# Optimization experiments

Hardware: AMD Instinct MI355X
Metric: run time of the kernel (lower is better)

The kernel has to match this reference:

```python
import jax, jax.numpy as jnp
import numpy as np

D_IN, D_HID = 64, 128

def _ff(x, w1, b1, w2, b2):
    # FeedForward: Linear -> ReLU -> Linear
    return jax.nn.relu(x @ w1 + b1) @ w2 + b2

def setup_inputs() -> dict:
    key = jax.random.key(0)
    ks = jax.random.split(key, 10)
    N, m = 8, 2048
    def lin(k, fan_in, fan_out):
        bound = 1.0 / np.sqrt(fan_in)
        return jax.random.uniform(k, (fan_in, fan_out), jnp.float32, -bound, bound)
    return {
        "x": jax.random.normal(ks[0], (N, m, D_IN), jnp.float32),
        "edge": jax.random.uniform(ks[1], (N, m, m), jnp.float32),
        # f: dim_in -> dim_hid//2 -> dim_hid
        "f_w1": lin(ks[2], D_IN, D_HID // 2),
        "f_b1": jnp.zeros((D_HID // 2,), jnp.float32),
        "f_w2": lin(ks[3], D_HID // 2, D_HID),
        "f_b2": jnp.zeros((D_HID,), jnp.float32),
        # g: 2*dim_in -> dim_hid -> dim_hid
        "g_w1": lin(ks[4], 2 * D_IN, D_HID),
        "g_b1": jnp.zeros((D_HID,), jnp.float32),
        "g_w2": lin(ks[5], D_HID, D_HID),
        "g_b2": jnp.zeros((D_HID,), jnp.float32),
    }

def reference(x, edge, f_w1, f_b1, f_w2, f_b2, g_w1, g_b1, g_w2, g_b2):
    # self dynamics: f(x) -> [N, m, D_HID]
    self_dyn = _ff(x, f_w1, f_b1, f_w2, f_b2)
    # Original builds interaction[n,i,j] = cat(x[n,i], x[n,i]) (receiver is
    # transposed twice), so g is constant along j. Compute g once per sender node.
    gx = _ff(jnp.concatenate([x, x], axis=-1), g_w1, g_b1, g_w2, g_b2)  # [N, m, H]
    # interaction.sum over sender dim i with edge weights: out[n,j] = sum_i edge[n,i,j]*gx[n,i]
    inter = jnp.einsum('nij,nih->njh', edge, gx)
    return self_dyn + inter
```

## Files before the change

kernel.cpp:

```cpp
#include <hip/hip_runtime.h>


typedef __attribute__((ext_vector_type(8))) short bf16x8;
typedef __attribute__((ext_vector_type(4))) unsigned short u16x4;
typedef __attribute__((ext_vector_type(4))) float f32x4;

static __device__ __forceinline__ unsigned short f2bf(float f) {
  union { float f; unsigned int i; } c; c.f = f;
  return (unsigned short)((c.i + 0x7fffu + ((c.i >> 16) & 1u)) >> 16);
}

__global__ __launch_bounds__(256) void k_gx(
    const float* __restrict__ x,
    const float* __restrict__ gw1,
    const float* __restrict__ gb1,
    const float* __restrict__ gw2,
    const float* __restrict__ gb2,
    unsigned short* __restrict__ gxT)
{
  __shared__ short xs[64 * 64];
  __shared__ short w1T[128 * 64];
  __shared__ short w2T[128 * 128];
  __shared__ short h2s[64 * 128];

  const int t = threadIdx.x;
  const int R0 = blockIdx.x * 64;

  for (int idx = t; idx < 64 * 128; idx += 256) {
    int k = idx >> 7, n = idx & 127;
    float v = gw1[idx] + gw1[64 * 128 + idx];
    w1T[(n << 6) + (((k >> 3) ^ (n & 7)) << 3) + (k & 7)] = (short)f2bf(v);
  }
  for (int idx = t; idx < 128 * 128; idx += 256) {
    int k = idx >> 7, n = idx & 127;
    w2T[(n << 7) + (((k >> 3) ^ (n & 7)) << 3) + (k & 7)] = (short)f2bf(gw2[idx]);
  }
  for (int s = t; s < 64 * 16; s += 256) {
    int row = s >> 4, c4 = s & 15;
    f32x4 v = *(const f32x4*)(x + (size_t)(R0 + row) * 64 + c4 * 4);
    u16x4 pk;
#pragma unroll
    for (int r = 0; r < 4; ++r) pk[r] = f2bf(v[r]);
    *(u16x4*)(xs + (row << 6) + (((c4 >> 1) ^ (row & 7)) << 3) + ((c4 & 1) << 2)) = pk;
  }
  __syncthreads();

  const int w = t >> 6, l = t & 63;
  const int lr = l & 15, q = l >> 4;
  const int mrow = w * 16 + lr;

  bf16x8 a[2];
#pragma unroll
  for (int ks = 0; ks < 2; ++ks) {
    int c = ks * 4 + q;
    a[ks] = *(const bf16x8*)(xs + (mrow << 6) + ((c ^ (mrow & 7)) << 3));
  }

  f32x4 acc;
#pragma unroll
  for (int nf = 0; nf < 8; ++nf) {
    acc = (f32x4){0.f, 0.f, 0.f, 0.f};
#pragma unroll
    for (int ks = 0; ks < 2; ++ks) {
      int c = ks * 4 + q;
      int nr = nf * 16 + lr;
      bf16x8 b = *(const bf16x8*)(w1T + (nr << 6) + ((c ^ (nr & 7)) << 3));
      acc = __builtin_amdgcn_mfma_f32_16x16x32_bf16(a[ks], b, acc, 0, 0, 0);
    }
    float bias = gb1[nf * 16 + lr];
#pragma unroll
    for (int r = 0; r < 4; ++r) {
      float v = acc[r] + bias;
      v = v > 0.f ? v : 0.f;
      int row = w * 16 + q * 4 + r, n = nf * 16 + lr;
      h2s[(row << 7) + (((n >> 3) ^ (row & 7)) << 3) + (n & 7)] = (short)f2bf(v);
    }
  }
  __syncthreads();

  bf16x8 a2[4];
#pragma unroll
  for (int ks = 0; ks < 4; ++ks) {
    int c = ks * 4 + q;
    a2[ks] = *(const bf16x8*)(h2s + (mrow << 7) + ((c ^ (mrow & 7)) << 3));
  }
  const int batch = R0 >> 11;
  const int ib = R0 & 2047;
#pragma unroll
  for (int nf = 0; nf < 8; ++nf) {
    acc = (f32x4){0.f, 0.f, 0.f, 0.f};
#pragma unroll
    for (int ks = 0; ks < 4; ++ks) {
      int c = ks * 4 + q;
      int nr = nf * 16 + lr;
      bf16x8 b = *(const bf16x8*)(w2T + (nr << 7) + ((c ^ (nr & 7)) << 3));
      acc = __builtin_amdgcn_mfma_f32_16x16x32_bf16(a2[ks], b, acc, 0, 0, 0);
    }
    float bias = gb2[nf * 16 + lr];
    u16x4 pk;
#pragma unroll
    for (int r = 0; r < 4; ++r) pk[r] = f2bf(acc[r] + bias);
    *(u16x4*)(gxT + (size_t)(batch * 128 + nf * 16 + lr) * 2048 + ib + w * 16 + q * 4) = pk;
  }
}

__global__ __launch_bounds__(256) void k_main(
    const float* __restrict__ edge,
    const unsigned short* __restrict__ gxT,
    const float* __restrict__ x,
    const float* __restrict__ fw1,
    const float* __restrict__ fb1,
    const float* __restrict__ fw2,
    const float* __restrict__ fb2,
    float* __restrict__ out)
{
  __shared__ short eT[2][32 * 72];
  __shared__ short bT[128 * 64];
  __shared__ short xs[32 * 64];
  __shared__ short w1T[64 * 64];
  __shared__ short h1s[32 * 64];

  const int t = threadIdx.x;
  const int batch = blockIdx.x & 7;
  const int j0 = (blockIdx.x >> 3) * 32;

  const int w = t >> 6, l = t & 63;
  const int wm = w & 1, wn = w >> 1;
  const int lr = l & 15, q = l >> 4;

  const int e_ii = t >> 2;
  const int e_cj = t & 3;

  const float* ep = edge + (size_t)batch * 2048 * 2048 + (size_t)e_ii * 2048 + j0 + e_cj * 8;
  const unsigned short* gp = gxT + ((size_t)batch * 128 + wn * 64 + lr) * 2048 + q * 8;

  f32x4 acc[4];
#pragma unroll
  for (int nf = 0; nf < 4; ++nf) acc[nf] = (f32x4){0.f, 0.f, 0.f, 0.f};

  auto lde = [&](int kk, f32x4 er[2]) {
    const float* p = ep + (size_t)kk * 64 * 2048;
    er[0] = __builtin_nontemporal_load((const f32x4*)p);
    er[1] = __builtin_nontemporal_load((const f32x4*)(p + 4));
  };
  auto ldg = [&](int kk, bf16x8 gf[8]) {
    const unsigned short* p = gp + kk * 64;
#pragma unroll
    for (int nf = 0; nf < 4; ++nf)
#pragma unroll
      for (int ks = 0; ks < 2; ++ks)
        gf[nf * 2 + ks] = *(const bf16x8*)(p + nf * 16 * 2048 + ks * 32);
  };
  auto st_e = [&](int buf, const f32x4 er[2]) {
#pragma unroll
    for (int u = 0; u < 8; ++u) {
      float v = (u < 4) ? er[0][u & 3] : er[1][u & 3];
      eT[buf][(e_cj * 8 + u) * 72 + (((e_ii >> 3) ^ e_cj) << 3) + (e_ii & 7)] = (short)f2bf(v);
    }
  };
  auto comp = [&](int buf, const bf16x8 gf[8]) {
#pragma unroll
    for (int ks = 0; ks < 2; ++ks) {
      const int c = ks * 4 + q;
      const int jj = wm * 16 + lr;
      bf16x8 a = *(const bf16x8*)(&eT[buf][jj * 72 + ((c ^ (jj >> 3)) << 3)]);
#pragma unroll
      for (int nf = 0; nf < 4; ++nf)
        acc[nf] = __builtin_amdgcn_mfma_f32_16x16x32_bf16(a, gf[nf * 2 + ks], acc[nf], 0, 0, 0);
    }
  };

  f32x4 erA[2], erB[2];
  bf16x8 gfA[8], gfB[8];

  lde(0, erA);
  ldg(0, gfA);
  lde(1, erB);
  st_e(0, erA);
  __syncthreads();

#pragma unroll 1
  for (int mm = 0; mm < 15; ++mm) {
    ldg(2 * mm + 1, gfB);
    lde(2 * mm + 2, erA);
    comp(0, gfA);
    st_e(1, erB);
    __syncthreads();
    ldg(2 * mm + 2, gfA);
    lde(2 * mm + 3, erB);
    comp(1, gfB);
    st_e(0, erA);
    __syncthreads();
  }
  ldg(31, gfB);
  comp(0, gfA);
  st_e(1, erB);
  __syncthreads();
  comp(1, gfB);

  for (int idx = t; idx < 64 * 64; idx += 256) {
    int k = idx >> 6, n = idx & 63;
    w1T[(n << 6) + (((k >> 3) ^ (n & 7)) << 3) + (k & 7)] = (short)f2bf(fw1[idx]);
  }
  for (int idx = t; idx < 64 * 128; idx += 256) {
    int k = idx >> 7, n = idx & 127;
    bT[(n << 6) + (((k >> 3) ^ (n & 7)) << 3) + (k & 7)] = (short)f2bf(fw2[idx]);
  }
  for (int s = t; s < 32 * 16; s += 256) {
    int row = s >> 4, c4 = s & 15;
    f32x4 v = *(const f32x4*)(x + (size_t)(batch * 2048 + j0 + row) * 64 + c4 * 4);
    u16x4 pk;
#pragma unroll
    for (int r = 0; r < 4; ++r) pk[r] = f2bf(v[r]);
    *(u16x4*)(xs + (row << 6) + (((c4 >> 1) ^ (row & 7)) << 3) + ((c4 & 1) << 2)) = pk;
  }
  __syncthreads();

  const int mrow = wm * 16 + lr;
  if (wn == 0) {
    bf16x8 a1[2];
#pragma unroll
    for (int ks = 0; ks < 2; ++ks) {
      int c = ks * 4 + q;
      a1[ks] = *(const bf16x8*)(xs + (mrow << 6) + ((c ^ (mrow & 7)) << 3));
    }
#pragma unroll
    for (int nf = 0; nf < 4; ++nf) {
      f32x4 h = (f32x4){0.f, 0.f, 0.f, 0.f};
#pragma unroll
      for (int ks = 0; ks < 2; ++ks) {
        int c = ks * 4 + q;
        int nr = nf * 16 + lr;
        bf16x8 b = *(const bf16x8*)(w1T + (nr << 6) + ((c ^ (nr & 7)) << 3));
        h = __builtin_amdgcn_mfma_f32_16x16x32_bf16(a1[ks], b, h, 0, 0, 0);
      }
      float bias = fb1[nf * 16 + lr];
#pragma unroll
      for (int r = 0; r < 4; ++r) {
        float v = h[r] + bias;
        v = v > 0.f ? v : 0.f;
        int row = wm * 16 + q * 4 + r, n = nf * 16 + lr;
        h1s[(row << 6) + (((n >> 3) ^ (row & 7)) << 3) + (n & 7)] = (short)f2bf(v);
      }
    }
  }
  __syncthreads();

  bf16x8 a2[2];
#pragma unroll
  for (int ks = 0; ks < 2; ++ks) {
    int c = ks * 4 + q;
    a2[ks] = *(const bf16x8*)(h1s + (mrow << 6) + ((c ^ (mrow & 7)) << 3));
  }
#pragma unroll
  for (int nf = 0; nf < 4; ++nf) {
    int h = wn * 64 + nf * 16 + lr;
#pragma unroll
    for (int ks = 0; ks < 2; ++ks) {
      int c = ks * 4 + q;
      bf16x8 b = *(const bf16x8*)(bT + (h << 6) + ((c ^ (h & 7)) << 3));
      acc[nf] = __builtin_amdgcn_mfma_f32_16x16x32_bf16(a2[ks], b, acc[nf], 0, 0, 0);
    }
    float bias = fb2[h];
#pragma unroll
    for (int r = 0; r < 4; ++r) {
      size_t o = ((size_t)batch * 2048 + j0 + wm * 16 + q * 4 + r) * 128 + h;
      out[o] = acc[nf][r] + bias;
    }
  }
}

extern "C" void kernel_launch(void* const* d_in, const int* in_sizes, int n_in,
                              void* d_out, int out_size, void* d_ws, size_t ws_size,
                              hipStream_t stream) {
  const float* x    = (const float*)d_in[0];
  const float* edge = (const float*)d_in[1];
  const float* fw1  = (const float*)d_in[2];
  const float* fb1  = (const float*)d_in[3];
  const float* fw2  = (const float*)d_in[4];
  const float* fb2  = (const float*)d_in[5];
  const float* gw1  = (const float*)d_in[6];
  const float* gb1  = (const float*)d_in[7];
  const float* gw2  = (const float*)d_in[8];
  const float* gb2  = (const float*)d_in[9];
  float* out = (float*)d_out;

  unsigned short* gxT = (unsigned short*)d_ws;

  hipLaunchKernelGGL(k_gx, dim3(256), dim3(256), 0, stream, x, gw1, gb1, gw2, gb2, gxT);
  hipLaunchKernelGGL(k_main, dim3(512), dim3(256), 0, stream, edge, gxT, x,
                     fw1, fb1, fw2, fb2, out);
}
```

Before: 280.5 us.

## Halve k_main column tile to 16 and double grid to 1024 blocks

Shrinks each k_main block's output tile from 32 to 16 columns, so the grid doubles to 1024 blocks. Warps are remapped so each covers 32 hidden channels of a single 16-row tile instead of a 2x2 split. Edge loads become one float4 per thread and drop the nontemporal hint, and launch bounds request 4 blocks per CU. The goal is more parallelism and occupancy for the edge-streaming GEMM on 256 CUs. The cost is that each block now reloads the full gxT slice and the f-MLP weights, which doubles gxT reads and setup work per output column.

```diff
diff --git a/kernel.cpp b/kernel.cpp
--- a/kernel.cpp
+++ b/kernel.cpp
@@ -104,7 +104,7 @@
   }
 }
 
-__global__ __launch_bounds__(256) void k_main(
+__global__ __launch_bounds__(256, 4) void k_main(
     const float* __restrict__ edge,
     const unsigned short* __restrict__ gxT,
     const float* __restrict__ x,
@@ -114,64 +114,60 @@
     const float* __restrict__ fb2,
     float* __restrict__ out)
 {
-  __shared__ short eT[2][32 * 72];
+  __shared__ short eT[2][16 * 72];
   __shared__ short bT[128 * 64];
-  __shared__ short xs[32 * 64];
+  __shared__ short xs[16 * 64];
   __shared__ short w1T[64 * 64];
-  __shared__ short h1s[32 * 64];
+  __shared__ short h1s[16 * 64];
 
   const int t = threadIdx.x;
   const int batch = blockIdx.x & 7;
-  const int j0 = (blockIdx.x >> 3) * 32;
+  const int j0 = (blockIdx.x >> 3) * 16;
 
   const int w = t >> 6, l = t & 63;
-  const int wm = w & 1, wn = w >> 1;
   const int lr = l & 15, q = l >> 4;
 
   const int e_ii = t >> 2;
   const int e_cj = t & 3;
 
-  const float* ep = edge + (size_t)batch * 2048 * 2048 + (size_t)e_ii * 2048 + j0 + e_cj * 8;
-  const unsigned short* gp = gxT + ((size_t)batch * 128 + wn * 64 + lr) * 2048 + q * 8;
-
-  f32x4 acc[4];
-#pragma unroll
-  for (int nf = 0; nf < 4; ++nf) acc[nf] = (f32x4){0.f, 0.f, 0.f, 0.f};
-
-  auto lde = [&](int kk, f32x4 er[2]) {
-    const float* p = ep + (size_t)kk * 64 * 2048;
-    er[0] = __builtin_nontemporal_load((const f32x4*)p);
-    er[1] = __builtin_nontemporal_load((const f32x4*)(p + 4));
-  };
-  auto ldg = [&](int kk, bf16x8 gf[8]) {
+  const float* ep = edge + (size_t)batch * 2048 * 2048 + (size_t)e_ii * 2048 + j0 + e_cj * 4;
+  const unsigned short* gp = gxT + ((size_t)batch * 128 + w * 32 + lr) * 2048 + q * 8;
+
+  f32x4 acc[2];
+#pragma unroll
+  for (int nf = 0; nf < 2; ++nf) acc[nf] = (f32x4){0.f, 0.f, 0.f, 0.f};
+
+  auto lde = [&](int kk, f32x4& er) {
+    er = *(const f32x4*)(ep + (size_t)kk * 64 * 2048);
+  };
+  auto ldg = [&](int kk, bf16x8 gf[4]) {
     const unsigned short* p = gp + kk * 64;
 #pragma unroll
-    for (int nf = 0; nf < 4; ++nf)
+    for (int nf = 0; nf < 2; ++nf)
 #pragma unroll
       for (int ks = 0; ks < 2; ++ks)
         gf[nf * 2 + ks] = *(const bf16x8*)(p + nf * 16 * 2048 + ks * 32);
   };
-  auto st_e = [&](int buf, const f32x4 er[2]) {
-#pragma unroll
-    for (int u = 0; u < 8; ++u) {
-      float v = (u < 4) ? er[0][u & 3] : er[1][u & 3];
-      eT[buf][(e_cj * 8 + u) * 72 + (((e_ii >> 3) ^ e_cj) << 3) + (e_ii & 7)] = (short)f2bf(v);
-    }
-  };
-  auto comp = [&](int buf, const bf16x8 gf[8]) {
+  auto st_e = [&](int buf, const f32x4& er) {
+#pragma unroll
+    for (int u = 0; u < 4; ++u) {
+      int jj = e_cj * 4 + u;
+      eT[buf][jj * 72 + (((e_ii >> 3) ^ (jj >> 3)) << 3) + (e_ii & 7)] = (short)f2bf(er[u]);
+    }
+  };
+  auto comp = [&](int buf, const bf16x8 gf[4]) {
 #pragma unroll
     for (int ks = 0; ks < 2; ++ks) {
       const int c = ks * 4 + q;
-      const int jj = wm * 16 + lr;
-      bf16x8 a = *(const bf16x8*)(&eT[buf][jj * 72 + ((c ^ (jj >> 3)) << 3)]);
-#pragma unroll
-      for (int nf = 0; nf < 4; ++nf)
+      bf16x8 a = *(const bf16x8*)(&eT[buf][lr * 72 + ((c ^ (lr >> 3)) << 3)]);
+#pragma unroll
+      for (int nf = 0; nf < 2; ++nf)
         acc[nf] = __builtin_amdgcn_mfma_f32_16x16x32_bf16(a, gf[nf * 2 + ks], acc[nf], 0, 0, 0);
     }
   };
 
-  f32x4 erA[2], erB[2];
-  bf16x8 gfA[8], gfB[8];
+  f32x4 erA, erB;
+  bf16x8 gfA[4], gfB[4];
 
   lde(0, erA);
   ldg(0, gfA);
@@ -206,7 +202,8 @@
     int k = idx >> 7, n = idx & 127;
     bT[(n << 6) + (((k >> 3) ^ (n & 7)) << 3) + (k & 7)] = (short)f2bf(fw2[idx]);
   }
-  for (int s = t; s < 32 * 16; s += 256) {
+  {
+    int s = t;
     int row = s >> 4, c4 = s & 15;
     f32x4 v = *(const f32x4*)(x + (size_t)(batch * 2048 + j0 + row) * 64 + c4 * 4);
     u16x4 pk;
@@ -216,13 +213,12 @@
   }
   __syncthreads();
 
-  const int mrow = wm * 16 + lr;
-  if (wn == 0) {
+  if (w == 0) {
     bf16x8 a1[2];
 #pragma unroll
     for (int ks = 0; ks < 2; ++ks) {
       int c = ks * 4 + q;
-      a1[ks] = *(const bf16x8*)(xs + (mrow << 6) + ((c ^ (mrow & 7)) << 3));
+      a1[ks] = *(const bf16x8*)(xs + (lr << 6) + ((c ^ (lr & 7)) << 3));
     }
 #pragma unroll
     for (int nf = 0; nf < 4; ++nf) {
@@ -239,7 +235,7 @@
       for (int r = 0; r < 4; ++r) {
         float v = h[r] + bias;
         v = v > 0.f ? v : 0.f;
-        int row = wm * 16 + q * 4 + r, n = nf * 16 + lr;
+        int row = q * 4 + r, n = nf * 16 + lr;
         h1s[(row << 6) + (((n >> 3) ^ (row & 7)) << 3) + (n & 7)] = (short)f2bf(v);
       }
     }
@@ -250,11 +246,11 @@
 #pragma unroll
   for (int ks = 0; ks < 2; ++ks) {
     int c = ks * 4 + q;
-    a2[ks] = *(const bf16x8*)(h1s + (mrow << 6) + ((c ^ (mrow & 7)) << 3));
-  }
-#pragma unroll
-  for (int nf = 0; nf < 4; ++nf) {
-    int h = wn * 64 + nf * 16 + lr;
+    a2[ks] = *(const bf16x8*)(h1s + (lr << 6) + ((c ^ (lr & 7)) << 3));
+  }
+#pragma unroll
+  for (int nf = 0; nf < 2; ++nf) {
+    int h = w * 32 + nf * 16 + lr;
 #pragma unroll
     for (int ks = 0; ks < 2; ++ks) {
       int c = ks * 4 + q;
@@ -264,7 +260,7 @@
     float bias = fb2[h];
 #pragma unroll
     for (int r = 0; r < 4; ++r) {
-      size_t o = ((size_t)batch * 2048 + j0 + wm * 16 + q * 4 + r) * 128 + h;
+      size_t o = ((size_t)batch * 2048 + j0 + q * 4 + r) * 128 + h;
       out[o] = acc[nf][r] + bias;
     }
   }
@@ -288,6 +284,6 @@
   unsigned short* gxT = (unsigned short*)d_ws;
 
   hipLaunchKernelGGL(k_gx, dim3(256), dim3(256), 0, stream, x, gw1, gb1, gw2, gb2, gxT);
-  hipLaunchKernelGGL(k_main, dim3(512), dim3(256), 0, stream, edge, gxT, x,
+  hipLaunchKernelGGL(k_main, dim3(1024), dim3(256), 0, stream, edge, gxT, x,
                      fw1, fb1, fw2, fb2, out);
 }
```

Result: no change. 281.4 us (+0.3%).

## Store gx in MFMA fragment order and repartition waves over output columns

Applied to the files above, without the earlier changes.

k_gx now writes gx in a pre-swizzled fragment layout, so each lane of k_main fetches contiguous 16-byte chunks of B operands instead of strided rows. k_main's wave split changes: each wave covers all 32 j rows and a 32-wide slice of hidden columns. This halves the per-wave gx register fragments, while each wave now reads two eT A-fragments per step. The change also drops nontemporal loads on edge and adds a launch_bounds occupancy hint of 2 blocks per CU. These target gx load traffic and register pressure, at the risk of extra LDS reads per wave.

```diff
diff --git a/kernel.cpp b/kernel.cpp
--- a/kernel.cpp
+++ b/kernel.cpp
@@ -16,7 +16,7 @@
     const float* __restrict__ gb1,
     const float* __restrict__ gw2,
     const float* __restrict__ gb2,
-    unsigned short* __restrict__ gxT)
+    unsigned short* __restrict__ gxF)
 {
   __shared__ short xs[64 * 64];
   __shared__ short w1T[128 * 64];
@@ -85,7 +85,10 @@
     a2[ks] = *(const bf16x8*)(h2s + (mrow << 7) + ((c ^ (mrow & 7)) << 3));
   }
   const int batch = R0 >> 11;
-  const int ib = R0 & 2047;
+  const int kk = (R0 & 2047) >> 6;
+  unsigned short* gbase = gxF + (size_t)batch * (128 * 2048) + (size_t)kk * (128 * 64);
+  const int cch = w * 2 + (q >> 1);
+  const int ks2 = cch >> 2, qq = cch & 3, r8 = (q & 1) * 4;
 #pragma unroll
   for (int nf = 0; nf < 8; ++nf) {
     acc = (f32x4){0.f, 0.f, 0.f, 0.f};
@@ -100,13 +103,13 @@
     u16x4 pk;
 #pragma unroll
     for (int r = 0; r < 4; ++r) pk[r] = f2bf(acc[r] + bias);
-    *(u16x4*)(gxT + (size_t)(batch * 128 + nf * 16 + lr) * 2048 + ib + w * 16 + q * 4) = pk;
+    *(u16x4*)(gbase + (((nf * 2 + ks2) * 64 + qq * 16 + lr) << 3) + r8) = pk;
   }
 }
 
-__global__ __launch_bounds__(256) void k_main(
+__global__ __launch_bounds__(256, 2) void k_main(
     const float* __restrict__ edge,
-    const unsigned short* __restrict__ gxT,
+    const unsigned short* __restrict__ gxF,
     const float* __restrict__ x,
     const float* __restrict__ fw1,
     const float* __restrict__ fb1,
@@ -125,53 +128,60 @@
   const int j0 = (blockIdx.x >> 3) * 32;
 
   const int w = t >> 6, l = t & 63;
-  const int wm = w & 1, wn = w >> 1;
   const int lr = l & 15, q = l >> 4;
 
   const int e_ii = t >> 2;
   const int e_cj = t & 3;
 
   const float* ep = edge + (size_t)batch * 2048 * 2048 + (size_t)e_ii * 2048 + j0 + e_cj * 8;
-  const unsigned short* gp = gxT + ((size_t)batch * 128 + wn * 64 + lr) * 2048 + q * 8;
+  const unsigned short* gp = gxF + (size_t)batch * (128 * 2048) + w * 2048 + (size_t)l * 8;
 
   f32x4 acc[4];
 #pragma unroll
-  for (int nf = 0; nf < 4; ++nf) acc[nf] = (f32x4){0.f, 0.f, 0.f, 0.f};
+  for (int i = 0; i < 4; ++i) acc[i] = (f32x4){0.f, 0.f, 0.f, 0.f};
 
   auto lde = [&](int kk, f32x4 er[2]) {
     const float* p = ep + (size_t)kk * 64 * 2048;
-    er[0] = __builtin_nontemporal_load((const f32x4*)p);
-    er[1] = __builtin_nontemporal_load((const f32x4*)(p + 4));
+    er[0] = *(const f32x4*)p;
+    er[1] = *(const f32x4*)(p + 4);
   };
-  auto ldg = [&](int kk, bf16x8 gf[8]) {
-    const unsigned short* p = gp + kk * 64;
-#pragma unroll
-    for (int nf = 0; nf < 4; ++nf)
+  auto ldg = [&](int kk, bf16x8 gf[4]) {
+    const unsigned short* p = gp + kk * 8192;
+#pragma unroll
+    for (int nf = 0; nf < 2; ++nf)
 #pragma unroll
       for (int ks = 0; ks < 2; ++ks)
-        gf[nf * 2 + ks] = *(const bf16x8*)(p + nf * 16 * 2048 + ks * 32);
+        gf[nf * 2 + ks] = *(const bf16x8*)(p + nf * 1024 + ks * 512);
   };
   auto st_e = [&](int buf, const f32x4 er[2]) {
 #pragma unroll
     for (int u = 0; u < 8; ++u) {
+      int jj = e_cj * 8 + u;
       float v = (u < 4) ? er[0][u & 3] : er[1][u & 3];
-      eT[buf][(e_cj * 8 + u) * 72 + (((e_ii >> 3) ^ e_cj) << 3) + (e_ii & 7)] = (short)f2bf(v);
+      eT[buf][jj * 72 + (((e_ii >> 3) ^ e_cj) << 3) + (e_ii & 7)] = (short)f2bf(v);
     }
   };
-  auto comp = [&](int buf, const bf16x8 gf[8]) {
+  auto comp = [&](int buf, const bf16x8 gf[4]) {
 #pragma unroll
     for (int ks = 0; ks < 2; ++ks) {
       const int c = ks * 4 + q;
-      const int jj = wm * 16 + lr;
-      bf16x8 a = *(const bf16x8*)(&eT[buf][jj * 72 + ((c ^ (jj >> 3)) << 3)]);
-#pragma unroll
-      for (int nf = 0; nf < 4; ++nf)
-        acc[nf] = __builtin_amdgcn_mfma_f32_16x16x32_bf16(a, gf[nf * 2 + ks], acc[nf], 0, 0, 0);
+      bf16x8 a[2];
+#pragma unroll
+      for (int jm = 0; jm < 2; ++jm) {
+        int jj = jm * 16 + lr;
+        a[jm] = *(const bf16x8*)(&eT[buf][jj * 72 + ((c ^ (jj >> 3)) << 3)]);
+      }
+#pragma unroll
+      for (int jm = 0; jm < 2; ++jm)
+#pragma unroll
+        for (int nf = 0; nf < 2; ++nf)
+          acc[jm * 2 + nf] = __builtin_amdgcn_mfma_f32_16x16x32_bf16(a[jm], gf[nf * 2 + ks],
+                                                                    acc[jm * 2 + nf], 0, 0, 0);
     }
   };
 
   f32x4 erA[2], erB[2];
-  bf16x8 gfA[8], gfB[8];
+  bf16x8 gfA[4], gfB[4];
 
   lde(0, erA);
   ldg(0, gfA);
@@ -216,8 +226,8 @@
   }
   __syncthreads();
 
-  const int mrow = wm * 16 + lr;
-  if (wn == 0) {
+  if (w < 2) {
+    const int mrow = w * 16 + lr;
     bf16x8 a1[2];
 #pragma unroll
     for (int ks = 0; ks < 2; ++ks) {
@@ -239,35 +249,41 @@
       for (int r = 0; r < 4; ++r) {
         float v = h[r] + bias;
         v = v > 0.f ? v : 0.f;
-        int row = wm * 16 + q * 4 + r, n = nf * 16 + lr;
+        int row = w * 16 + q * 4 + r, n = nf * 16 + lr;
         h1s[(row << 6) + (((n >> 3) ^ (row & 7)) << 3) + (n & 7)] = (short)f2bf(v);
       }
     }
   }
   __syncthreads();
 
-  bf16x8 a2[2];
-#pragma unroll
-  for (int ks = 0; ks < 2; ++ks) {
-    int c = ks * 4 + q;
-    a2[ks] = *(const bf16x8*)(h1s + (mrow << 6) + ((c ^ (mrow & 7)) << 3));
-  }
-#pragma unroll
-  for (int nf = 0; nf < 4; ++nf) {
-    int h = wn * 64 + nf * 16 + lr;
+  bf16x8 a2[2][2];
+#pragma unroll
+  for (int jm = 0; jm < 2; ++jm)
 #pragma unroll
     for (int ks = 0; ks < 2; ++ks) {
       int c = ks * 4 + q;
-      bf16x8 b = *(const bf16x8*)(bT + (h << 6) + ((c ^ (h & 7)) << 3));
-      acc[nf] = __builtin_amdgcn_mfma_f32_16x16x32_bf16(a2[ks], b, acc[nf], 0, 0, 0);
-    }
-    float bias = fb2[h];
-#pragma unroll
-    for (int r = 0; r < 4; ++r) {
-      size_t o = ((size_t)batch * 2048 + j0 + wm * 16 + q * 4 + r) * 128 + h;
-      out[o] = acc[nf][r] + bias;
-    }
-  }
+      int mrow = jm * 16 + lr;
+      a2[jm][ks] = *(const bf16x8*)(h1s + (mrow << 6) + ((c ^ (mrow & 7)) << 3));
+    }
+#pragma unroll
+  for (int jm = 0; jm < 2; ++jm)
+#pragma unroll
+    for (int nf = 0; nf < 2; ++nf) {
+      int h = w * 32 + nf * 16 + lr;
+#pragma unroll
+      for (int ks = 0; ks < 2; ++ks) {
+        int c = ks * 4 + q;
+        bf16x8 b = *(const bf16x8*)(bT + (h << 6) + ((c ^ (h & 7)) << 3));
+        acc[jm * 2 + nf] = __builtin_amdgcn_mfma_f32_16x16x32_bf16(a2[jm][ks], b,
+                                                                  acc[jm * 2 + nf], 0, 0, 0);
+      }
+      float bias = fb2[h];
+#pragma unroll
+      for (int r = 0; r < 4; ++r) {
+        size_t o = ((size_t)batch * 2048 + j0 + jm * 16 + q * 4 + r) * 128 + h;
+        out[o] = acc[jm * 2 + nf][r] + bias;
+      }
+    }
 }
 
 extern "C" void kernel_launch(void* const* d_in, const int* in_sizes, int n_in,
@@ -285,9 +301,9 @@
   const float* gb2  = (const float*)d_in[9];
   float* out = (float*)d_out;
 
-  unsigned short* gxT = (unsigned short*)d_ws;
-
-  hipLaunchKernelGGL(k_gx, dim3(256), dim3(256), 0, stream, x, gw1, gb1, gw2, gb2, gxT);
-  hipLaunchKernelGGL(k_main, dim3(512), dim3(256), 0, stream, edge, gxT, x,
+  unsigned short* gxF = (unsigned short*)d_ws;
+
+  hipLaunchKernelGGL(k_gx, dim3(256), dim3(256), 0, stream, x, gw1, gb1, gw2, gb2, gxF);
+  hipLaunchKernelGGL(k_main, dim3(512), dim3(256), 0, stream, edge, gxF, x,
                      fw1, fb1, fw2, fb2, out);
 }
```

After: 244.8 us. 1.15x faster.
